# Kernel tuning notes

Hardware: AMD Instinct MI355X
Metric: run time of the kernel (lower is better)

## Reference

```python
import jax, jax.numpy as jnp
import numpy as np

B, S, E = 8, 1024, 1024
H, HS = 16, 64  # num_heads, head_size; H*HS == E


def setup_inputs() -> dict:
    key = jax.random.key(0)
    ks = jax.random.split(key, 6)
    scale = 1.0 / np.sqrt(E)
    x = jax.random.normal(ks[0], (B, S, E), dtype=jnp.float32)
    # per-head projection weights stacked: [H, E, HS] (Linear(n_embd, head_size, bias=False))
    Wq = jax.random.normal(ks[1], (H, E, HS), dtype=jnp.float32) * scale
    Wk = jax.random.normal(ks[2], (H, E, HS), dtype=jnp.float32) * scale
    Wv = jax.random.normal(ks[3], (H, E, HS), dtype=jnp.float32) * scale
    # output projection Linear(n_embd, n_embd): torch weight [out, in] plus bias
    Wproj = jax.random.normal(ks[4], (E, E), dtype=jnp.float32) * scale
    bproj = jax.random.normal(ks[5], (E,), dtype=jnp.float32) * scale
    return {"x": x, "Wq": Wq, "Wk": Wk, "Wv": Wv, "Wproj": Wproj, "bproj": bproj}


def reference(x, Wq, Wk, Wv, Wproj, bproj):
    # q,k,v: [B, H, S, HS]
    q = jnp.einsum('bse,hed->bhsd', x, Wq)
    k = jnp.einsum('bse,hed->bhsd', x, Wk)
    v = jnp.einsum('bse,hed->bhsd', x, Wv)
    scores = jnp.einsum('bhsd,bhtd->bhst', q, k) * (HS ** -0.5)  # [B,H,S,S]
    causal = jnp.tril(jnp.ones((S, S), dtype=bool))
    scores = jnp.where(causal, scores, jnp.finfo(scores.dtype).min)
    attn = jax.nn.softmax(scores, axis=-1)
    out = jnp.einsum('bhst,bhtd->bhsd', attn, v)         # [B,H,S,HS]
    out = out.transpose(0, 2, 1, 3).reshape(B, S, H * HS)  # concat heads -> [B,S,E]
    return out @ Wproj.T + bproj  # dropout p=0 is identity
```

## Files before the change

kernel.cpp:

```cpp
#include <hip/hip_runtime.h>
#include <stdint.h>

#define DEVI __device__ __forceinline__

typedef __attribute__((ext_vector_type(8))) short bf16x8;
typedef __attribute__((ext_vector_type(4))) float floatx4;
typedef __attribute__((ext_vector_type(16))) float floatx16;

constexpr int Bb = 8, Ss = 1024, Ee = 1024, Hh = 16, HSs = 64;
constexpr int Mq = Bb * Ss;
constexpr int Nqkv = 3 * Hh * HSs;
constexpr int Kd = Ee;

DEVI unsigned short f2bf(float x) {
  union { float f; uint32_t u; } v; v.f = x;
  uint32_t r = v.u + 0x7FFFu + ((v.u >> 16) & 1u);
  return (unsigned short)(r >> 16);
}

DEVI uint32_t pk2(float a, float b) {
  return (uint32_t)f2bf(a) | ((uint32_t)f2bf(b) << 16);
}

DEVI bf16x8 mkfrag(uint32_t a, uint32_t b, uint32_t c, uint32_t d) {
  union { uint32_t u[4]; bf16x8 v; } x;
  x.u[0] = a; x.u[1] = b; x.u[2] = c; x.u[3] = d;
  return x.v;
}

DEVI floatx4 mfma16(bf16x8 a, bf16x8 b, floatx4 c) {
  return __builtin_amdgcn_mfma_f32_16x16x32_bf16(a, b, c, 0, 0, 0);
}
DEVI floatx16 mfma32(bf16x8 a, bf16x8 b, floatx16 c) {
  return __builtin_amdgcn_mfma_f32_32x32x16_bf16(a, b, c, 0, 0, 0);
}

DEVI void gload_lds16(const void* g, void* l) {
  __builtin_amdgcn_global_load_lds(
      (const __attribute__((address_space(1))) uint32_t*)(uintptr_t)g,
      (__attribute__((address_space(3))) uint32_t*)(uint32_t)(uintptr_t)l,
      16, 0, 0);
}

__global__ void cvt_f32_bf16(const float* __restrict__ in, unsigned short* __restrict__ out, int n) {
  int i = (blockIdx.x * blockDim.x + threadIdx.x) * 4;
  if (i >= n) return;
  float4 v = *(const float4*)&in[i];
  ushort4 o;
  o.x = f2bf(v.x); o.y = f2bf(v.y); o.z = f2bf(v.z); o.w = f2bf(v.w);
  *(ushort4*)(void*)&out[i] = o;
}

__global__ void cvt_wqkv(const float* __restrict__ Wq, const float* __restrict__ Wk,
                         const float* __restrict__ Wv, unsigned short* __restrict__ out) {
  __shared__ float tile[64][65];
  const int k0 = blockIdx.x * 64;
  const int hh = blockIdx.y;
  const int qkv = hh >> 4, h = hh & 15;
  const float* W = (qkv == 0) ? Wq : ((qkv == 1) ? Wk : Wv);
  const float scale = (qkv == 0) ? (0.125f * 1.44269504f) : 1.0f;
  const float* src = W + (size_t)h * Ee * HSs;
  const int c = threadIdx.x & 63, r4 = threadIdx.x >> 6;
#pragma unroll
  for (int rr = 0; rr < 16; ++rr) {
    int row = rr * 4 + r4;
    tile[row][c] = src[(size_t)(k0 + row) * HSs + c] * scale;
  }
  __syncthreads();
  const int base_n = qkv * 1024 + h * 64;
#pragma unroll
  for (int rr = 0; rr < 16; ++rr) {
    int hs = rr * 4 + r4;
    out[(size_t)(base_n + hs) * Kd + k0 + c] = f2bf(tile[c][hs]);
  }
}

template <int EPI>
__global__ __launch_bounds__(256, 2) void gemm_bt(
    const unsigned short* __restrict__ A, const unsigned short* __restrict__ Bt,
    unsigned short* __restrict__ Qb, unsigned short* __restrict__ Kb,
    unsigned short* __restrict__ Vtb, float* __restrict__ Out,
    const float* __restrict__ bias, int Mdim, int Ndim, int Kdim) {
  __shared__ __align__(16) unsigned short As[128 * 64];
  __shared__ __align__(16) unsigned short Bs[128 * 64];
  const int tid = threadIdx.x;
  const int lane = tid & 63;
  const int wid = tid >> 6;
  const int wm = wid >> 1, wn = wid & 1;
  const int m0 = blockIdx.y * 128;
  const int n0 = blockIdx.x * 128;

  floatx4 acc[4][4];
#pragma unroll
  for (int i = 0; i < 4; ++i)
#pragma unroll
    for (int j = 0; j < 4; ++j) acc[i][j] = (floatx4)0.f;

  const int srow = lane >> 3;
  const int schunk = (lane & 7) ^ srow;

  for (int kt = 0; kt < Kdim; kt += 64) {
#pragma unroll
    for (int j = 0; j < 4; ++j) {
      const int g = wid * 4 + j;
      const int row = g * 8 + srow;
      gload_lds16(A + (size_t)(m0 + row) * Kdim + kt + schunk * 8, &As[g * 8 * 64]);
      gload_lds16(Bt + (size_t)(n0 + row) * Kdim + kt + schunk * 8, &Bs[g * 8 * 64]);
    }
    __syncthreads();
#pragma unroll
    for (int kk = 0; kk < 2; ++kk) {
      const int c = kk * 4 + (lane >> 4);
      bf16x8 af[4], bf[4];
#pragma unroll
      for (int i = 0; i < 4; ++i) {
        const int ra = wm * 64 + i * 16 + (lane & 15);
        af[i] = *(const bf16x8*)&As[ra * 64 + ((c ^ (ra & 7)) << 3)];
        const int rb = wn * 64 + i * 16 + (lane & 15);
        bf[i] = *(const bf16x8*)&Bs[rb * 64 + ((c ^ (rb & 7)) << 3)];
      }
#pragma unroll
      for (int i = 0; i < 4; ++i)
#pragma unroll
        for (int j = 0; j < 4; ++j) acc[i][j] = mfma16(af[i], bf[j], acc[i][j]);
    }
    __syncthreads();
  }

  const int mrow0 = m0 + wm * 64 + ((lane >> 4) << 2);
  const int ncol0 = n0 + wn * 64 + (lane & 15);
  if (EPI == 0) {
#pragma unroll
    for (int i = 0; i < 4; ++i) {
#pragma unroll
      for (int j = 0; j < 4; ++j) {
        const int n = ncol0 + j * 16;
        const int qkv = n >> 10;
        const int h = (n & 1023) >> 6;
        const int hs = n & 63;
#pragma unroll
        for (int r = 0; r < 4; ++r) {
          const int m = mrow0 + i * 16 + r;
          const int b = m >> 10, s = m & 1023;
          const unsigned short bv = f2bf(acc[i][j][r]);
          if (qkv == 0)
            Qb[(((size_t)b * Hh + h) * Ss + s) * HSs + hs] = bv;
          else if (qkv == 1)
            Kb[(((size_t)b * Hh + h) * Ss + s) * HSs + hs] = bv;
          else
            Vtb[(((size_t)b * Hh + h) * HSs + hs) * Ss + s] = bv;
        }
      }
    }
  } else {
#pragma unroll
    for (int j = 0; j < 4; ++j) {
      const int n = ncol0 + j * 16;
      const float bj = bias[n];
#pragma unroll
      for (int i = 0; i < 4; ++i) {
#pragma unroll
        for (int r = 0; r < 4; ++r) {
          const int m = mrow0 + i * 16 + r;
          Out[(size_t)m * Ndim + n] = acc[i][j][r] + bj;
        }
      }
    }
  }
}

__global__ __launch_bounds__(256, 3) void attn(
    const unsigned short* __restrict__ Qb, const unsigned short* __restrict__ Kb,
    const unsigned short* __restrict__ Vtb, unsigned short* __restrict__ Ob) {
  __shared__ __align__(16) unsigned short Ks[64 * 64];
  __shared__ __align__(16) unsigned short Vs[64 * 64];

  const int tid = threadIdx.x;
  const int lane = tid & 63;
  const int wid = tid >> 6;
  const int ln = lane & 31;
  const int hi = lane >> 5;
  const int bh = blockIdx.y;
  const int q0 = (gridDim.x - 1 - blockIdx.x) * 128;
  const int bI = bh >> 4, hI = bh & 15;
  const unsigned short* Qp = Qb + (size_t)bh * Ss * HSs;
  const unsigned short* Kp = Kb + (size_t)bh * Ss * HSs;
  const unsigned short* Vp = Vtb + (size_t)bh * HSs * Ss;
  const int qw = q0 + wid * 32;
  const int q = qw + ln;

  bf16x8 qf[4];
#pragma unroll
  for (int kc = 0; kc < 4; ++kc)
    qf[kc] = *(const bf16x8*)&Qp[(size_t)q * 64 + kc * 16 + hi * 8];

  floatx16 oacc[2];
  oacc[0] = (floatx16)0.f;
  oacc[1] = (floatx16)0.f;
  float mrow = -3.0e38f, lrow = 0.f;

  const int srow = lane >> 3;
  const int schunk = (lane & 7) ^ srow;
  const int ntiles = (q0 >> 6) + 2;

  for (int t = 0; t < ntiles; ++t) {
    const int t0 = t * 64;
#pragma unroll
    for (int j = 0; j < 2; ++j) {
      const int g = wid * 2 + j;
      const int row = g * 8 + srow;
      gload_lds16(Kp + (size_t)(t0 + row) * 64 + schunk * 8, &Ks[g * 8 * 64]);
      gload_lds16(Vp + (size_t)row * Ss + t0 + schunk * 8, &Vs[g * 8 * 64]);
    }
    __syncthreads();

    if (t0 <= qw + 31) {
      floatx16 sc[2];
#pragma unroll
      for (int tt = 0; tt < 2; ++tt) {
        floatx16 s = (floatx16)0.f;
#pragma unroll
        for (int kc = 0; kc < 4; ++kc) {
          const int row = tt * 32 + ln;
          bf16x8 kf = *(const bf16x8*)&Ks[row * 64 + ((((kc << 1) | hi) ^ (ln & 7)) << 3)];
          s = mfma32(kf, qf[kc], s);
        }
        sc[tt] = s;
      }
      if (t0 + 63 > qw) {
#pragma unroll
        for (int tt = 0; tt < 2; ++tt)
#pragma unroll
          for (int r = 0; r < 16; ++r) {
            const int tg = t0 + tt * 32 + (r & 3) + 8 * (r >> 2) + 4 * hi;
            if (tg > q) sc[tt][r] = -1e30f;
          }
      }
      float mx = sc[0][0];
#pragma unroll
      for (int tt = 0; tt < 2; ++tt)
#pragma unroll
        for (int r = 0; r < 16; ++r) mx = fmaxf(mx, sc[tt][r]);
      mx = fmaxf(mx, __shfl_xor(mx, 32));
      const float mnew = fmaxf(mrow, mx);
      const float scal = __builtin_amdgcn_exp2f(mrow - mnew);
      mrow = mnew;
      float ss = 0.f;
#pragma unroll
      for (int tt = 0; tt < 2; ++tt)
#pragma unroll
        for (int r = 0; r < 16; ++r) {
          const float p = __builtin_amdgcn_exp2f(sc[tt][r] - mnew);
          sc[tt][r] = p;
          ss += p;
        }
      ss += __shfl_xor(ss, 32);
      lrow = lrow * scal + ss;
#pragma unroll
      for (int dt = 0; dt < 2; ++dt)
#pragma unroll
        for (int r = 0; r < 16; ++r) oacc[dt][r] *= scal;

      bf16x8 pf[4];
#pragma unroll
      for (int tt = 0; tt < 2; ++tt)
#pragma unroll
        for (int fb = 0; fb < 2; ++fb) {
          const int b = fb * 8;
          const uint32_t w0 = pk2(sc[tt][b + 0], sc[tt][b + 1]);
          const uint32_t w1 = pk2(sc[tt][b + 2], sc[tt][b + 3]);
          const uint32_t w2 = pk2(sc[tt][b + 4], sc[tt][b + 5]);
          const uint32_t w3 = pk2(sc[tt][b + 6], sc[tt][b + 7]);
          const uint32_t x0 = (uint32_t)__shfl_xor((int)w0, 32);
          const uint32_t x1 = (uint32_t)__shfl_xor((int)w1, 32);
          const uint32_t x2 = (uint32_t)__shfl_xor((int)w2, 32);
          const uint32_t x3 = (uint32_t)__shfl_xor((int)w3, 32);
          pf[tt * 2 + fb] = mkfrag(hi ? x2 : w0, hi ? x3 : w1, hi ? w2 : x0, hi ? w3 : x1);
        }
#pragma unroll
      for (int dt = 0; dt < 2; ++dt) {
        const int row = dt * 32 + ln;
#pragma unroll
        for (int kc = 0; kc < 4; ++kc) {
          bf16x8 vf = *(const bf16x8*)&Vs[row * 64 + ((((kc << 1) | hi) ^ (ln & 7)) << 3)];
          oacc[dt] = mfma32(vf, pf[kc], oacc[dt]);
        }
      }
    }
    __syncthreads();
  }

  const float inv = 1.0f / lrow;
  unsigned short* Op = Ob + ((size_t)bI * Ss + q) * Ee + hI * 64;
#pragma unroll
  for (int dt = 0; dt < 2; ++dt)
#pragma unroll
    for (int g4 = 0; g4 < 4; ++g4) {
      ushort4 o;
      o.x = f2bf(oacc[dt][g4 * 4 + 0] * inv);
      o.y = f2bf(oacc[dt][g4 * 4 + 1] * inv);
      o.z = f2bf(oacc[dt][g4 * 4 + 2] * inv);
      o.w = f2bf(oacc[dt][g4 * 4 + 3] * inv);
      *(ushort4*)(void*)&Op[dt * 32 + g4 * 8 + hi * 4] = o;
    }
}

extern "C" void kernel_launch(void* const* d_in, const int* in_sizes, int n_in,
                              void* d_out, int out_size, void* d_ws, size_t ws_size,
                              hipStream_t stream) {
  const float* x = (const float*)d_in[0];
  const float* Wq = (const float*)d_in[1];
  const float* Wk = (const float*)d_in[2];
  const float* Wv = (const float*)d_in[3];
  const float* Wproj = (const float*)d_in[4];
  const float* bproj = (const float*)d_in[5];
  float* out = (float*)d_out;

  char* ws = (char*)d_ws;
  unsigned short* xb     = (unsigned short*)(ws);
  unsigned short* wqkvb  = (unsigned short*)(ws + (16u << 20));
  unsigned short* wprojb = (unsigned short*)(ws + (22u << 20));
  unsigned short* Qb     = (unsigned short*)(ws + (24u << 20));
  unsigned short* Kb     = (unsigned short*)(ws + (40u << 20));
  unsigned short* Vtb    = (unsigned short*)(ws + (56u << 20));
  unsigned short* Obuf   = (unsigned short*)(ws + (72u << 20));

  cvt_f32_bf16<<<8192, 256, 0, stream>>>(x, xb, Bb * Ss * Ee);
  cvt_wqkv<<<dim3(16, 48), 256, 0, stream>>>(Wq, Wk, Wv, wqkvb);
  cvt_f32_bf16<<<1024, 256, 0, stream>>>(Wproj, wprojb, Ee * Ee);
  gemm_bt<0><<<dim3(Nqkv / 128, Mq / 128), 256, 0, stream>>>(
      xb, wqkvb, Qb, Kb, Vtb, nullptr, nullptr, Mq, Nqkv, Kd);
  attn<<<dim3(Ss / 128, Bb * Hh), 256, 0, stream>>>(Qb, Kb, Vtb, Obuf);
  gemm_bt<1><<<dim3(Ee / 128, Mq / 128), 256, 0, stream>>>(
      Obuf, wprojb, nullptr, nullptr, nullptr, out, bproj, Mq, Ee, Kd);
}
```

Baseline: 180.0 us.

## Triple-buffer GEMM and attention LDS loads with interleaved prefetch and priority hints

```diff
diff --git a/kernel.cpp b/kernel.cpp
--- a/kernel.cpp
+++ b/kernel.cpp
@@ -2,6 +2,7 @@
 #include <stdint.h>
 
 #define DEVI __device__ __forceinline__
+#define SBAR() __builtin_amdgcn_s_barrier()
 
 typedef __attribute__((ext_vector_type(8))) short bf16x8;
 typedef __attribute__((ext_vector_type(4))) float floatx4;
@@ -76,55 +77,115 @@
 }
 
 template <int EPI>
-__global__ __launch_bounds__(256, 2) void gemm_bt(
+__global__ __launch_bounds__(512, 2) void gemm_bt(
     const unsigned short* __restrict__ A, const unsigned short* __restrict__ Bt,
     unsigned short* __restrict__ Qb, unsigned short* __restrict__ Kb,
     unsigned short* __restrict__ Vtb, float* __restrict__ Out,
     const float* __restrict__ bias, int Mdim, int Ndim, int Kdim) {
-  __shared__ __align__(16) unsigned short As[128 * 64];
-  __shared__ __align__(16) unsigned short Bs[128 * 64];
+  __shared__ __align__(16) unsigned short As[3][128 * 64];
+  __shared__ __align__(16) unsigned short Bs[3][256 * 64];
   const int tid = threadIdx.x;
   const int lane = tid & 63;
   const int wid = tid >> 6;
-  const int wm = wid >> 1, wn = wid & 1;
+  const int wm = wid >> 2, wn = wid & 3;
   const int m0 = blockIdx.y * 128;
-  const int n0 = blockIdx.x * 128;
-
-  floatx4 acc[4][4];
-#pragma unroll
-  for (int i = 0; i < 4; ++i)
-#pragma unroll
-    for (int j = 0; j < 4; ++j) acc[i][j] = (floatx4)0.f;
-
+  const int n0 = blockIdx.x * 256;
   const int srow = lane >> 3;
   const int schunk = (lane & 7) ^ srow;
-
-  for (int kt = 0; kt < Kdim; kt += 64) {
-#pragma unroll
-    for (int j = 0; j < 4; ++j) {
-      const int g = wid * 4 + j;
+  const int NT = Kdim >> 6;
+
+  floatx4 acc[4][4];
+#pragma unroll
+  for (int i = 0; i < 4; ++i)
+#pragma unroll
+    for (int j = 0; j < 4; ++j) acc[i][j] = (floatx4)0.f;
+
+  auto stageA = [&](int kt, int b) {
+#pragma unroll
+    for (int i = 0; i < 2; ++i) {
+      const int g = wid + i * 8;
       const int row = g * 8 + srow;
-      gload_lds16(A + (size_t)(m0 + row) * Kdim + kt + schunk * 8, &As[g * 8 * 64]);
-      gload_lds16(Bt + (size_t)(n0 + row) * Kdim + kt + schunk * 8, &Bs[g * 8 * 64]);
-    }
-    __syncthreads();
-#pragma unroll
-    for (int kk = 0; kk < 2; ++kk) {
-      const int c = kk * 4 + (lane >> 4);
-      bf16x8 af[4], bf[4];
-#pragma unroll
-      for (int i = 0; i < 4; ++i) {
-        const int ra = wm * 64 + i * 16 + (lane & 15);
-        af[i] = *(const bf16x8*)&As[ra * 64 + ((c ^ (ra & 7)) << 3)];
-        const int rb = wn * 64 + i * 16 + (lane & 15);
-        bf[i] = *(const bf16x8*)&Bs[rb * 64 + ((c ^ (rb & 7)) << 3)];
-      }
-#pragma unroll
-      for (int i = 0; i < 4; ++i)
-#pragma unroll
-        for (int j = 0; j < 4; ++j) acc[i][j] = mfma16(af[i], bf[j], acc[i][j]);
-    }
-    __syncthreads();
+      gload_lds16(A + (size_t)(m0 + row) * Kdim + kt * 64 + schunk * 8, &As[b][g * 512]);
+    }
+  };
+  auto stageB = [&](int kt, int b, int half) {
+#pragma unroll
+    for (int i = 0; i < 2; ++i) {
+      const int g = half * 16 + wid + i * 8;
+      const int row = g * 8 + srow;
+      gload_lds16(Bt + (size_t)(n0 + row) * Kdim + kt * 64 + schunk * 8, &Bs[b][g * 512]);
+    }
+  };
+
+  stageA(0, 0); stageB(0, 0, 0); stageB(0, 0, 1);
+  stageA(1, 1); stageB(1, 1, 0); stageB(1, 1, 1);
+  asm volatile("s_waitcnt vmcnt(6)" ::: "memory");
+  SBAR();
+
+  for (int kt = 0; kt < NT; ++kt) {
+    const int cur = kt % 3;
+    const int nx2 = (kt + 2) % 3;
+    const bool pf = (kt + 2 < NT);
+    const unsigned short* Ab = As[cur];
+    const unsigned short* Bb = Bs[cur];
+    bf16x8 bf[4][2], af[2];
+
+#pragma unroll
+    for (int nj = 0; nj < 4; ++nj) {
+      const int rb = wn * 64 + nj * 16 + (lane & 15);
+#pragma unroll
+      for (int kk = 0; kk < 2; ++kk) {
+        const int c = kk * 4 + (lane >> 4);
+        bf[nj][kk] = *(const bf16x8*)&Bb[rb * 64 + ((c ^ (rb & 7)) << 3)];
+      }
+    }
+    {
+      const int ra = wm * 64 + 0 * 16 + (lane & 15);
+#pragma unroll
+      for (int kk = 0; kk < 2; ++kk) {
+        const int c = kk * 4 + (lane >> 4);
+        af[kk] = *(const bf16x8*)&Ab[ra * 64 + ((c ^ (ra & 7)) << 3)];
+      }
+    }
+    if (pf) stageA(kt + 2, nx2);
+    SBAR();
+    __builtin_amdgcn_s_setprio(1);
+#pragma unroll
+    for (int nj = 0; nj < 4; ++nj) {
+      acc[0][nj] = mfma16(af[0], bf[nj][0], acc[0][nj]);
+      acc[0][nj] = mfma16(af[1], bf[nj][1], acc[0][nj]);
+    }
+    __builtin_amdgcn_s_setprio(0);
+    SBAR();
+
+#pragma unroll
+    for (int mi = 1; mi < 4; ++mi) {
+      {
+        const int ra = wm * 64 + mi * 16 + (lane & 15);
+#pragma unroll
+        for (int kk = 0; kk < 2; ++kk) {
+          const int c = kk * 4 + (lane >> 4);
+          af[kk] = *(const bf16x8*)&Ab[ra * 64 + ((c ^ (ra & 7)) << 3)];
+        }
+      }
+      if (mi == 1) {
+        if (pf) stageB(kt + 2, nx2, 0);
+      } else if (mi == 2) {
+        if (pf) stageB(kt + 2, nx2, 1);
+      } else {
+        if (pf) { asm volatile("s_waitcnt vmcnt(6)" ::: "memory"); }
+        else    { asm volatile("s_waitcnt vmcnt(0)" ::: "memory"); }
+      }
+      SBAR();
+      __builtin_amdgcn_s_setprio(1);
+#pragma unroll
+      for (int nj = 0; nj < 4; ++nj) {
+        acc[mi][nj] = mfma16(af[0], bf[nj][0], acc[mi][nj]);
+        acc[mi][nj] = mfma16(af[1], bf[nj][1], acc[mi][nj]);
+      }
+      __builtin_amdgcn_s_setprio(0);
+      SBAR();
+    }
   }
 
   const int mrow0 = m0 + wm * 64 + ((lane >> 4) << 2);
@@ -172,8 +233,8 @@
 __global__ __launch_bounds__(256, 3) void attn(
     const unsigned short* __restrict__ Qb, const unsigned short* __restrict__ Kb,
     const unsigned short* __restrict__ Vtb, unsigned short* __restrict__ Ob) {
-  __shared__ __align__(16) unsigned short Ks[64 * 64];
-  __shared__ __align__(16) unsigned short Vs[64 * 64];
+  __shared__ __align__(16) unsigned short Ks[3][64 * 64];
+  __shared__ __align__(16) unsigned short Vs[3][64 * 64];
 
   const int tid = threadIdx.x;
   const int lane = tid & 63;
@@ -201,30 +262,44 @@
 
   const int srow = lane >> 3;
   const int schunk = (lane & 7) ^ srow;
-  const int ntiles = (q0 >> 6) + 2;
-
-  for (int t = 0; t < ntiles; ++t) {
-    const int t0 = t * 64;
+  const int nt = (q0 >> 6) + 2;
+
+  auto stageKV = [&](int t, int b) {
 #pragma unroll
     for (int j = 0; j < 2; ++j) {
       const int g = wid * 2 + j;
       const int row = g * 8 + srow;
-      gload_lds16(Kp + (size_t)(t0 + row) * 64 + schunk * 8, &Ks[g * 8 * 64]);
-      gload_lds16(Vp + (size_t)row * Ss + t0 + schunk * 8, &Vs[g * 8 * 64]);
-    }
-    __syncthreads();
+      gload_lds16(Kp + (size_t)(t * 64 + row) * 64 + schunk * 8, &Ks[b][g * 512]);
+      gload_lds16(Vp + (size_t)row * Ss + t * 64 + schunk * 8, &Vs[b][g * 512]);
+    }
+  };
+
+  stageKV(0, 0);
+  stageKV(1, 1);
+  asm volatile("s_waitcnt vmcnt(4)" ::: "memory");
+  SBAR();
+
+  for (int t = 0; t < nt; ++t) {
+    const int cur = t % 3;
+    const bool pf = (t + 2 < nt);
+    if (pf) stageKV(t + 2, (t + 2) % 3);
+    const int t0 = t * 64;
 
     if (t0 <= qw + 31) {
+      const unsigned short* Kc = Ks[cur];
+      const unsigned short* Vc = Vs[cur];
       floatx16 sc[2];
 #pragma unroll
       for (int tt = 0; tt < 2; ++tt) {
         floatx16 s = (floatx16)0.f;
+        __builtin_amdgcn_s_setprio(1);
 #pragma unroll
         for (int kc = 0; kc < 4; ++kc) {
           const int row = tt * 32 + ln;
-          bf16x8 kf = *(const bf16x8*)&Ks[row * 64 + ((((kc << 1) | hi) ^ (ln & 7)) << 3)];
+          bf16x8 kf = *(const bf16x8*)&Kc[row * 64 + ((((kc << 1) | hi) ^ (ln & 7)) << 3)];
           s = mfma32(kf, qf[kc], s);
         }
+        __builtin_amdgcn_s_setprio(0);
         sc[tt] = s;
       }
       if (t0 + 63 > qw) {
@@ -261,7 +336,7 @@
 #pragma unroll
         for (int r = 0; r < 16; ++r) oacc[dt][r] *= scal;
 
-      bf16x8 pf[4];
+      bf16x8 pf_[4];
 #pragma unroll
       for (int tt = 0; tt < 2; ++tt)
 #pragma unroll
@@ -275,19 +350,24 @@
           const uint32_t x1 = (uint32_t)__shfl_xor((int)w1, 32);
           const uint32_t x2 = (uint32_t)__shfl_xor((int)w2, 32);
           const uint32_t x3 = (uint32_t)__shfl_xor((int)w3, 32);
-          pf[tt * 2 + fb] = mkfrag(hi ? x2 : w0, hi ? x3 : w1, hi ? w2 : x0, hi ? w3 : x1);
+          pf_[tt * 2 + fb] = mkfrag(hi ? x2 : w0, hi ? x3 : w1, hi ? w2 : x0, hi ? w3 : x1);
         }
 #pragma unroll
       for (int dt = 0; dt < 2; ++dt) {
         const int row = dt * 32 + ln;
+        __builtin_amdgcn_s_setprio(1);
 #pragma unroll
         for (int kc = 0; kc < 4; ++kc) {
-          bf16x8 vf = *(const bf16x8*)&Vs[row * 64 + ((((kc << 1) | hi) ^ (ln & 7)) << 3)];
-          oacc[dt] = mfma32(vf, pf[kc], oacc[dt]);
-        }
-      }
-    }
-    __syncthreads();
+          bf16x8 vf = *(const bf16x8*)&Vc[row * 64 + ((((kc << 1) | hi) ^ (ln & 7)) << 3)];
+          oacc[dt] = mfma32(vf, pf_[kc], oacc[dt]);
+        }
+        __builtin_amdgcn_s_setprio(0);
+      }
+    }
+
+    if (pf) { asm volatile("s_waitcnt vmcnt(4)" ::: "memory"); }
+    else    { asm volatile("s_waitcnt vmcnt(0)" ::: "memory"); }
+    SBAR();
   }
 
   const float inv = 1.0f / lrow;
@@ -328,9 +408,9 @@
   cvt_f32_bf16<<<8192, 256, 0, stream>>>(x, xb, Bb * Ss * Ee);
   cvt_wqkv<<<dim3(16, 48), 256, 0, stream>>>(Wq, Wk, Wv, wqkvb);
   cvt_f32_bf16<<<1024, 256, 0, stream>>>(Wproj, wprojb, Ee * Ee);
-  gemm_bt<0><<<dim3(Nqkv / 128, Mq / 128), 256, 0, stream>>>(
+  gemm_bt<0><<<dim3(Nqkv / 256, Mq / 128), 512, 0, stream>>>(
       xb, wqkvb, Qb, Kb, Vtb, nullptr, nullptr, Mq, Nqkv, Kd);
   attn<<<dim3(Ss / 128, Bb * Hh), 256, 0, stream>>>(Qb, Kb, Vtb, Obuf);
-  gemm_bt<1><<<dim3(Ee / 128, Mq / 128), 256, 0, stream>>>(
+  gemm_bt<1><<<dim3(Ee / 256, Mq / 128), 512, 0, stream>>>(
       Obuf, wprojb, nullptr, nullptr, nullptr, out, bproj, Mq, Ee, Kd);
 }
```

Result: slower. 207.0 us (+15.0%).

## Multi-buffer LDS loads in GEMM and attention, enlarge attention blocks

Applied to the files above, without the earlier changes.

```diff
diff --git a/kernel.cpp b/kernel.cpp
--- a/kernel.cpp
+++ b/kernel.cpp
@@ -81,33 +81,42 @@
     unsigned short* __restrict__ Qb, unsigned short* __restrict__ Kb,
     unsigned short* __restrict__ Vtb, float* __restrict__ Out,
     const float* __restrict__ bias, int Mdim, int Ndim, int Kdim) {
-  __shared__ __align__(16) unsigned short As[128 * 64];
-  __shared__ __align__(16) unsigned short Bs[128 * 64];
+  __shared__ __align__(16) unsigned short As[2][128 * 64];
+  __shared__ __align__(16) unsigned short Bs[2][128 * 64];
   const int tid = threadIdx.x;
   const int lane = tid & 63;
   const int wid = tid >> 6;
   const int wm = wid >> 1, wn = wid & 1;
   const int m0 = blockIdx.y * 128;
   const int n0 = blockIdx.x * 128;
-
-  floatx4 acc[4][4];
-#pragma unroll
-  for (int i = 0; i < 4; ++i)
-#pragma unroll
-    for (int j = 0; j < 4; ++j) acc[i][j] = (floatx4)0.f;
-
   const int srow = lane >> 3;
   const int schunk = (lane & 7) ^ srow;
-
-  for (int kt = 0; kt < Kdim; kt += 64) {
+  const int NT = Kdim >> 6;
+
+  floatx4 acc[4][4];
+#pragma unroll
+  for (int i = 0; i < 4; ++i)
+#pragma unroll
+    for (int j = 0; j < 4; ++j) acc[i][j] = (floatx4)0.f;
+
+  auto stage = [&](int kt, int b) {
 #pragma unroll
     for (int j = 0; j < 4; ++j) {
       const int g = wid * 4 + j;
       const int row = g * 8 + srow;
-      gload_lds16(A + (size_t)(m0 + row) * Kdim + kt + schunk * 8, &As[g * 8 * 64]);
-      gload_lds16(Bt + (size_t)(n0 + row) * Kdim + kt + schunk * 8, &Bs[g * 8 * 64]);
-    }
-    __syncthreads();
+      gload_lds16(A + (size_t)(m0 + row) * Kdim + kt * 64 + schunk * 8, &As[b][g * 512]);
+      gload_lds16(Bt + (size_t)(n0 + row) * Kdim + kt * 64 + schunk * 8, &Bs[b][g * 512]);
+    }
+  };
+
+  stage(0, 0);
+  __syncthreads();
+
+  for (int kt = 0; kt < NT; ++kt) {
+    const int cur = kt & 1;
+    if (kt + 1 < NT) stage(kt + 1, cur ^ 1);
+    const unsigned short* Ap = As[cur];
+    const unsigned short* Bp = Bs[cur];
 #pragma unroll
     for (int kk = 0; kk < 2; ++kk) {
       const int c = kk * 4 + (lane >> 4);
@@ -115,9 +124,9 @@
 #pragma unroll
       for (int i = 0; i < 4; ++i) {
         const int ra = wm * 64 + i * 16 + (lane & 15);
-        af[i] = *(const bf16x8*)&As[ra * 64 + ((c ^ (ra & 7)) << 3)];
+        af[i] = *(const bf16x8*)&Ap[ra * 64 + ((c ^ (ra & 7)) << 3)];
         const int rb = wn * 64 + i * 16 + (lane & 15);
-        bf[i] = *(const bf16x8*)&Bs[rb * 64 + ((c ^ (rb & 7)) << 3)];
+        bf[i] = *(const bf16x8*)&Bp[rb * 64 + ((c ^ (rb & 7)) << 3)];
       }
 #pragma unroll
       for (int i = 0; i < 4; ++i)
@@ -169,19 +178,20 @@
   }
 }
 
-__global__ __launch_bounds__(256, 3) void attn(
+__global__ __launch_bounds__(512, 4) void attn(
     const unsigned short* __restrict__ Qb, const unsigned short* __restrict__ Kb,
     const unsigned short* __restrict__ Vtb, unsigned short* __restrict__ Ob) {
-  __shared__ __align__(16) unsigned short Ks[64 * 64];
-  __shared__ __align__(16) unsigned short Vs[64 * 64];
+  __shared__ __align__(16) unsigned short Ks[3][64 * 64];
+  __shared__ __align__(16) unsigned short Vs[3][64 * 64];
 
   const int tid = threadIdx.x;
   const int lane = tid & 63;
   const int wid = tid >> 6;
   const int ln = lane & 31;
   const int hi = lane >> 5;
-  const int bh = blockIdx.y;
-  const int q0 = (gridDim.x - 1 - blockIdx.x) * 128;
+  const int bh = blockIdx.x & 127;
+  const int qs = blockIdx.x >> 7;
+  const int q0 = (3 - qs) * 256;
   const int bI = bh >> 4, hI = bh & 15;
   const unsigned short* Qp = Qb + (size_t)bh * Ss * HSs;
   const unsigned short* Kp = Kb + (size_t)bh * Ss * HSs;
@@ -201,30 +211,40 @@
 
   const int srow = lane >> 3;
   const int schunk = (lane & 7) ^ srow;
-  const int ntiles = (q0 >> 6) + 2;
-
-  for (int t = 0; t < ntiles; ++t) {
+  const int nt = (q0 >> 6) + 4;
+
+  auto stageKV = [&](int t, int b) {
+    const int row = wid * 8 + srow;
+    gload_lds16(Kp + (size_t)(t * 64 + row) * 64 + schunk * 8, &Ks[b][wid * 512]);
+    gload_lds16(Vp + (size_t)row * Ss + t * 64 + schunk * 8, &Vs[b][wid * 512]);
+  };
+
+  stageKV(0, 0);
+  stageKV(1, 1);
+  asm volatile("s_waitcnt vmcnt(2)" ::: "memory");
+  __builtin_amdgcn_s_barrier();
+
+  for (int t = 0; t < nt; ++t) {
+    const int cur = t % 3;
+    const bool pf = (t + 2 < nt);
+    if (pf) stageKV(t + 2, (t + 2) % 3);
     const int t0 = t * 64;
-#pragma unroll
-    for (int j = 0; j < 2; ++j) {
-      const int g = wid * 2 + j;
-      const int row = g * 8 + srow;
-      gload_lds16(Kp + (size_t)(t0 + row) * 64 + schunk * 8, &Ks[g * 8 * 64]);
-      gload_lds16(Vp + (size_t)row * Ss + t0 + schunk * 8, &Vs[g * 8 * 64]);
-    }
-    __syncthreads();
 
     if (t0 <= qw + 31) {
+      const unsigned short* Kc = Ks[cur];
+      const unsigned short* Vc = Vs[cur];
       floatx16 sc[2];
 #pragma unroll
       for (int tt = 0; tt < 2; ++tt) {
         floatx16 s = (floatx16)0.f;
+        __builtin_amdgcn_s_setprio(1);
 #pragma unroll
         for (int kc = 0; kc < 4; ++kc) {
           const int row = tt * 32 + ln;
-          bf16x8 kf = *(const bf16x8*)&Ks[row * 64 + ((((kc << 1) | hi) ^ (ln & 7)) << 3)];
+          bf16x8 kf = *(const bf16x8*)&Kc[row * 64 + ((((kc << 1) | hi) ^ (ln & 7)) << 3)];
           s = mfma32(kf, qf[kc], s);
         }
+        __builtin_amdgcn_s_setprio(0);
         sc[tt] = s;
       }
       if (t0 + 63 > qw) {
@@ -261,7 +281,7 @@
 #pragma unroll
         for (int r = 0; r < 16; ++r) oacc[dt][r] *= scal;
 
-      bf16x8 pf[4];
+      bf16x8 pf_[4];
 #pragma unroll
       for (int tt = 0; tt < 2; ++tt)
 #pragma unroll
@@ -275,19 +295,24 @@
           const uint32_t x1 = (uint32_t)__shfl_xor((int)w1, 32);
           const uint32_t x2 = (uint32_t)__shfl_xor((int)w2, 32);
           const uint32_t x3 = (uint32_t)__shfl_xor((int)w3, 32);
-          pf[tt * 2 + fb] = mkfrag(hi ? x2 : w0, hi ? x3 : w1, hi ? w2 : x0, hi ? w3 : x1);
+          pf_[tt * 2 + fb] = mkfrag(hi ? x2 : w0, hi ? x3 : w1, hi ? w2 : x0, hi ? w3 : x1);
         }
 #pragma unroll
       for (int dt = 0; dt < 2; ++dt) {
         const int row = dt * 32 + ln;
+        __builtin_amdgcn_s_setprio(1);
 #pragma unroll
         for (int kc = 0; kc < 4; ++kc) {
-          bf16x8 vf = *(const bf16x8*)&Vs[row * 64 + ((((kc << 1) | hi) ^ (ln & 7)) << 3)];
-          oacc[dt] = mfma32(vf, pf[kc], oacc[dt]);
-        }
-      }
-    }
-    __syncthreads();
+          bf16x8 vf = *(const bf16x8*)&Vc[row * 64 + ((((kc << 1) | hi) ^ (ln & 7)) << 3)];
+          oacc[dt] = mfma32(vf, pf_[kc], oacc[dt]);
+        }
+        __builtin_amdgcn_s_setprio(0);
+      }
+    }
+
+    if (pf) { asm volatile("s_waitcnt vmcnt(2)" ::: "memory"); }
+    else    { asm volatile("s_waitcnt vmcnt(0)" ::: "memory"); }
+    __builtin_amdgcn_s_barrier();
   }
 
   const float inv = 1.0f / lrow;
@@ -330,7 +355,7 @@
   cvt_f32_bf16<<<1024, 256, 0, stream>>>(Wproj, wprojb, Ee * Ee);
   gemm_bt<0><<<dim3(Nqkv / 128, Mq / 128), 256, 0, stream>>>(
       xb, wqkvb, Qb, Kb, Vtb, nullptr, nullptr, Mq, Nqkv, Kd);
-  attn<<<dim3(Ss / 128, Bb * Hh), 256, 0, stream>>>(Qb, Kb, Vtb, Obuf);
+  attn<<<512, 512, 0, stream>>>(Qb, Kb, Vtb, Obuf);
   gemm_bt<1><<<dim3(Ee / 128, Mq / 128), 256, 0, stream>>>(
       Obuf, wprojb, nullptr, nullptr, nullptr, out, bproj, Mq, Ee, Kd);
 }
```

Result: faster. 167.5 us (-7.0%).
